# Kernel tuning notes

Measured on AMD Instinct MI355X. Metric: run time of the kernel, lower is better.

## Reference

```python
import jax, jax.numpy as jnp
import numpy as np

N_NODES = 50000
N_FEAT = 128
HIDDEN = 3
N_EDGES = 600000
N_POWERS = 3


def setup_inputs() -> dict:
    key = jax.random.key(0)
    ks = jax.random.split(key, 6)
    x = jax.random.normal(ks[0], (N_NODES, N_FEAT), dtype=jnp.float32)
    edge_index = jax.random.randint(ks[1], (N_POWERS, 2, N_EDGES), 0, N_NODES, dtype=jnp.int64)
    # MLP params for the 3 adjacency powers, stacked on the leading axis.
    # torch Linear(in,out) stored transposed here: y = x @ W + b.
    Wa = jax.random.normal(ks[2], (N_POWERS, N_FEAT, HIDDEN), dtype=jnp.float32) * (1.0 / np.sqrt(N_FEAT))
    ba = jax.random.normal(ks[3], (N_POWERS, HIDDEN), dtype=jnp.float32) * 0.01
    Wb = jax.random.normal(ks[4], (N_POWERS, HIDDEN, 1), dtype=jnp.float32) * (1.0 / np.sqrt(HIDDEN))
    bb = jax.random.normal(ks[5], (N_POWERS, 1), dtype=jnp.float32) * 0.01
    return {"x": x, "edge_index": edge_index, "Wa": Wa, "ba": ba, "Wb": Wb, "bb": bb}


def reference(x, edge_index, Wa, ba, Wb, bb):
    # Gather source/target node features per edge, per adjacency power.
    x_j = x[edge_index[:, 0]]          # [P, E, F]
    x_i = x[edge_index[:, 1]]          # [P, E, F]
    abs_dif = jnp.abs(x_j - x_i)       # [P, E, F]
    # Tiny per-edge MLP: Linear -> ReLU -> Linear -> Sigmoid (separate params per power).
    h = jax.nn.relu(jnp.einsum('pef,pfh->peh', abs_dif, Wa) + ba[:, None, :])  # [P, E, H]
    w = jax.nn.sigmoid(jnp.einsum('peh,pho->peo', h, Wb) + bb[:, None, :])     # [P, E, 1]
    return w[..., 0]                   # [P, E] edge weights for each power
```

## Files before the change

kernel.cpp:

```cpp
#include <hip/hip_runtime.h>
#include <math.h>

#define N_NODES 50000
#define N_FEAT  128
#define N_EDGES 600000
#define N_POWERS 3

#define PAIRS 5
#define EDGES_PER_BLK (64 * PAIRS)

#define CAP 81920
#define NBUCK 8
#define CHUNK 2048
#define NCHUNK 293

typedef _Float16 half2v __attribute__((ext_vector_type(2)));
union HU { unsigned u; half2v h; };

__device__ __forceinline__ int bucket_of(int j) { return (int)(((unsigned)j * 41u) >> 18); }

__global__ __launch_bounds__(256) void conv_x_plain(const float* __restrict__ x,
                                                    unsigned* __restrict__ xh,
                                                    const float* __restrict__ Wa,
                                                    unsigned* __restrict__ wah) {
    const int t = blockIdx.x * 256 + threadIdx.x;
    const float4* x4 = (const float4*)x;
    float4 a = x4[(size_t)t * 2];
    float4 b = x4[(size_t)t * 2 + 1];
    HU p0, p1, p2, p3;
    p0.h = half2v{(_Float16)a.x, (_Float16)a.y};
    p1.h = half2v{(_Float16)a.z, (_Float16)a.w};
    p2.h = half2v{(_Float16)b.x, (_Float16)b.y};
    p3.h = half2v{(_Float16)b.z, (_Float16)b.w};
    ((uint4*)xh)[t] = uint4{p0.u, p1.u, p2.u, p3.u};
    if (blockIdx.x == 0 && threadIdx.x < 192) {
        const int tt = threadIdx.x;
        #pragma unroll
        for (int q = 0; q < 3; ++q) {
            int idx = tt + q * 192;
            int c  = idx % 3;
            int pk = idx / 3;
            int k  = pk % 64;
            int p  = pk / 64;
            float w0 = Wa[p * 384 + (2 * k) * 3 + c];
            float w1 = Wa[p * 384 + (2 * k + 1) * 3 + c];
            HU u; u.h = half2v{(_Float16)w0, (_Float16)w1};
            wah[idx] = u.u;
        }
    }
}

__global__ __launch_bounds__(256) void hist_kernel(const int* __restrict__ edge_index,
                                                   int* __restrict__ hist) {
    __shared__ int lh[NBUCK];
    const int p = blockIdx.y, chunk = blockIdx.x;
    if (threadIdx.x < NBUCK) lh[threadIdx.x] = 0;
    __syncthreads();
    const int* ej = edge_index + (size_t)p * 2 * N_EDGES;
    const int base = chunk * CHUNK;
    #pragma unroll
    for (int k = 0; k < 8; ++k) {
        const int e = base + k * 256 + threadIdx.x;
        if (e < N_EDGES) {
            const int j = __builtin_nontemporal_load(ej + e);
            atomicAdd(&lh[bucket_of(j)], 1);
        }
    }
    __syncthreads();
    if (threadIdx.x < NBUCK)
        hist[(p * NBUCK + threadIdx.x) * NCHUNK + chunk] = lh[threadIdx.x];
}

__global__ __launch_bounds__(64) void scan_hist(int* __restrict__ hist,
                                                int* __restrict__ cur) {
    const int pb = blockIdx.x;
    const int lane = threadIdx.x;
    int* h = hist + pb * NCHUNK;
    int carry = 0;
    for (int t = 0; t < NCHUNK; t += 64) {
        const int c = t + lane;
        int v = (c < NCHUNK) ? h[c] : 0;
        int s = v;
        #pragma unroll
        for (int d = 1; d < 64; d <<= 1) {
            int u = __shfl_up(s, d, 64);
            if (lane >= d) s += u;
        }
        if (c < NCHUNK) h[c] = carry + (s - v);
        carry += __shfl(s, 63, 64);
    }
    if (lane == 0) cur[pb] = carry;
}

__global__ __launch_bounds__(256) void scatter_pass(const int* __restrict__ edge_index,
                                                    const int* __restrict__ hist,
                                                    unsigned long long* __restrict__ su) {
    __shared__ int lc[NBUCK];
    const int p = blockIdx.y, chunk = blockIdx.x;
    if (threadIdx.x < NBUCK) lc[threadIdx.x] = 0;
    __syncthreads();
    const int* ej = edge_index + (size_t)p * 2 * N_EDGES;
    const int* ei = ej + N_EDGES;
    const int base = chunk * CHUNK;
    #pragma unroll
    for (int k = 0; k < 8; ++k) {
        const int e = base + k * 256 + threadIdx.x;
        if (e < N_EDGES) {
            const int j = __builtin_nontemporal_load(ej + e);
            const int i = __builtin_nontemporal_load(ei + e);
            const int b = bucket_of(j);
            const int pos = atomicAdd(&lc[b], 1);
            const int off = hist[(p * NBUCK + b) * NCHUNK + chunk];
            const size_t slot = (size_t)(p * NBUCK + b) * CAP + off + pos;
            su[slot] = (unsigned long long)(unsigned)(j | (i << 16))
                     | ((unsigned long long)e << 32);
        }
    }
}

template<int PAT>
__device__ __forceinline__ float swz(float v) {
    return __int_as_float(__builtin_amdgcn_ds_swizzle(__float_as_int(v), PAT));
}

__device__ __forceinline__ void dot3_8(const uint4& qa0, const uint4& qa1,
                                       const uint4& qb0, const uint4& qb1,
                                       const HU wa[8][3],
                                       float& h0, float& h1, float& h2) {
    unsigned ua[8] = {qa0.x, qa0.y, qa0.z, qa0.w, qa1.x, qa1.y, qa1.z, qa1.w};
    unsigned ub[8] = {qb0.x, qb0.y, qb0.z, qb0.w, qb1.x, qb1.y, qb1.z, qb1.w};
    h0 = 0.f; h1 = 0.f; h2 = 0.f;
    #pragma unroll
    for (int k = 0; k < 8; ++k) {
        HU a, b, d;
        a.u = ua[k]; b.u = ub[k];
        d.h = a.h - b.h;
        d.u &= 0x7fff7fffu;
        h0 = __builtin_amdgcn_fdot2(d.h, wa[k][0].h, h0, false);
        h1 = __builtin_amdgcn_fdot2(d.h, wa[k][1].h, h1, false);
        h2 = __builtin_amdgcn_fdot2(d.h, wa[k][2].h, h2, false);
    }
}

__global__ __launch_bounds__(256) void adj_kernel_sorted(
    const unsigned* __restrict__ xh,
    const unsigned long long* __restrict__ su,
    const int* __restrict__ cur,
    const unsigned* __restrict__ wah,
    const float* __restrict__ ba,
    const float* __restrict__ Wb,
    const float* __restrict__ bb,
    float* __restrict__ out)
{
    const int p    = blockIdx.y;
    const int b    = blockIdx.x & 7;
    const int k    = blockIdx.x >> 3;
    const int tid  = threadIdx.x;
    const int lane = tid & 63;
    const int wave = tid >> 6;
    const int sub  = lane & 7;
    const int grp  = lane >> 3;

    const int count = cur[p * NBUCK + b];
    const int base  = k * EDGES_PER_BLK;
    if (base >= count) return;

    HU wa[8][3];
    {
        const unsigned* wp = wah + ((size_t)p * 64 + sub * 8) * 3;
        #pragma unroll
        for (int kk = 0; kk < 8; ++kk) {
            wa[kk][0].u = wp[kk * 3 + 0];
            wa[kk][1].u = wp[kk * 3 + 1];
            wa[kk][2].u = wp[kk * 3 + 2];
        }
        #pragma unroll
        for (int kk = 0; kk < 8; ++kk) {
            asm volatile("" : "+v"(wa[kk][0].u), "+v"(wa[kk][1].u), "+v"(wa[kk][2].u));
        }
    }

    const float ba0 = ba[p * 3 + 0], ba1 = ba[p * 3 + 1], ba2 = ba[p * 3 + 2];
    const float wb0 = Wb[p * 3 + 0], wb1 = Wb[p * 3 + 1], wb2 = Wb[p * 3 + 2];
    const float bbp = bb[p];

    const unsigned long long* sup = su + (size_t)(p * NBUCK + b) * CAP;
    float* outp = out + (size_t)p * N_EDGES;

    const int eoff = wave * 8 + grp;
    const int roff = sub * 8;
    const int cm1  = count - 1;

    #pragma unroll
    for (int it = 0; it < PAIRS; ++it) {
        const int r1 = base + it * 64 + eoff;
        const int r2 = r1 + 32;
        const bool v1 = r1 < count;
        const bool v2 = r2 < count;
        const int s1 = min(r1, cm1);
        const int s2 = min(r2, cm1);

        const unsigned long long q1 = __builtin_nontemporal_load(sup + s1);
        const unsigned long long q2 = __builtin_nontemporal_load(sup + s2);
        const int j1 = (int)(q1 & 0xFFFFu);
        const int i1 = (int)((q1 >> 16) & 0xFFFFu);
        const int e1 = (int)(q1 >> 32);
        const int j2 = (int)(q2 & 0xFFFFu);
        const int i2 = (int)((q2 >> 16) & 0xFFFFu);
        const int e2 = (int)(q2 >> 32);

        const uint4* rj1 = (const uint4*)(xh + ((size_t)j1 << 6) + roff);
        const uint4* ri1 = (const uint4*)(xh + ((size_t)i1 << 6) + roff);
        const uint4* rj2 = (const uint4*)(xh + ((size_t)j2 << 6) + roff);
        const uint4* ri2 = (const uint4*)(xh + ((size_t)i2 << 6) + roff);
        uint4 a0 = rj1[0], a1 = rj1[1];
        uint4 b0 = ri1[0], b1 = ri1[1];
        uint4 c0 = rj2[0], c1 = rj2[1];
        uint4 d0 = ri2[0], d1 = ri2[1];

        float h0a, h1a, h2a, h0b, h1b, h2b;
        dot3_8(a0, a1, b0, b1, wa, h0a, h1a, h2a);
        dot3_8(c0, c1, d0, d1, wa, h0b, h1b, h2b);

        h0a += swz<0x041F>(h0a); h1a += swz<0x041F>(h1a); h2a += swz<0x041F>(h2a);
        h0b += swz<0x041F>(h0b); h1b += swz<0x041F>(h1b); h2b += swz<0x041F>(h2b);
        h0a += swz<0x081F>(h0a); h1a += swz<0x081F>(h1a); h2a += swz<0x081F>(h2a);
        h0b += swz<0x081F>(h0b); h1b += swz<0x081F>(h1b); h2b += swz<0x081F>(h2b);
        h0a += swz<0x101F>(h0a); h1a += swz<0x101F>(h1a); h2a += swz<0x101F>(h2a);
        h0b += swz<0x101F>(h0b); h1b += swz<0x101F>(h1b); h2b += swz<0x101F>(h2b);

        if (sub == 0) {
            if (v1) {
                float r0 = fmaxf(h0a + ba0, 0.f);
                float r1f = fmaxf(h1a + ba1, 0.f);
                float r2f = fmaxf(h2a + ba2, 0.f);
                float s  = fmaf(r0, wb0, fmaf(r1f, wb1, fmaf(r2f, wb2, bbp)));
                __builtin_nontemporal_store(1.f / (1.f + __expf(-s)), outp + e1);
            }
            if (v2) {
                float r0 = fmaxf(h0b + ba0, 0.f);
                float r1f = fmaxf(h1b + ba1, 0.f);
                float r2f = fmaxf(h2b + ba2, 0.f);
                float s  = fmaf(r0, wb0, fmaf(r1f, wb1, fmaf(r2f, wb2, bbp)));
                __builtin_nontemporal_store(1.f / (1.f + __expf(-s)), outp + e2);
            }
        }
    }
}

__global__ __launch_bounds__(256) void adj_kernel_f16(
    const unsigned* __restrict__ xh,
    const unsigned* __restrict__ wah,
    const int*   __restrict__ edge_index,
    const float* __restrict__ ba,
    const float* __restrict__ Wb,
    const float* __restrict__ bb,
    float* __restrict__ out)
{
    const int p    = blockIdx.y;
    const int tid  = threadIdx.x;
    const int lane = tid & 63;
    const int wave = tid >> 6;
    const int sub  = lane & 7;
    const int grp  = lane >> 3;

    HU wa[8][3];
    {
        const unsigned* wp = wah + ((size_t)p * 64 + sub * 8) * 3;
        #pragma unroll
        for (int k = 0; k < 8; ++k) {
            wa[k][0].u = wp[k * 3 + 0];
            wa[k][1].u = wp[k * 3 + 1];
            wa[k][2].u = wp[k * 3 + 2];
        }
        #pragma unroll
        for (int k = 0; k < 8; ++k) {
            asm volatile("" : "+v"(wa[k][0].u), "+v"(wa[k][1].u), "+v"(wa[k][2].u));
        }
    }

    const float ba0 = ba[p * 3 + 0], ba1 = ba[p * 3 + 1], ba2 = ba[p * 3 + 2];
    const float wb0 = Wb[p * 3 + 0], wb1 = Wb[p * 3 + 1], wb2 = Wb[p * 3 + 2];
    const float bbp = bb[p];

    const int* ej = edge_index + (size_t)p * 2 * N_EDGES;
    const int* ei = ej + N_EDGES;
    float* outp = out + (size_t)p * N_EDGES;

    const int e_blk = blockIdx.x * EDGES_PER_BLK;
    const int eoff  = wave * 8 + grp;
    const int roff  = sub * 8;

    #pragma unroll
    for (int it = 0; it < PAIRS; ++it) {
        const int e1 = e_blk + it * 64 + eoff;
        const int e2 = e1 + 32;
        const int j1 = __builtin_nontemporal_load(ej + e1);
        const int i1 = __builtin_nontemporal_load(ei + e1);
        const int j2 = __builtin_nontemporal_load(ej + e2);
        const int i2 = __builtin_nontemporal_load(ei + e2);

        const uint4* rj1 = (const uint4*)(xh + ((size_t)j1 << 6) + roff);
        const uint4* ri1 = (const uint4*)(xh + ((size_t)i1 << 6) + roff);
        const uint4* rj2 = (const uint4*)(xh + ((size_t)j2 << 6) + roff);
        const uint4* ri2 = (const uint4*)(xh + ((size_t)i2 << 6) + roff);
        uint4 a0 = rj1[0], a1 = rj1[1];
        uint4 b0 = ri1[0], b1 = ri1[1];
        uint4 c0 = rj2[0], c1 = rj2[1];
        uint4 d0 = ri2[0], d1 = ri2[1];

        float h0a, h1a, h2a, h0b, h1b, h2b;
        dot3_8(a0, a1, b0, b1, wa, h0a, h1a, h2a);
        dot3_8(c0, c1, d0, d1, wa, h0b, h1b, h2b);

        h0a += swz<0x041F>(h0a); h1a += swz<0x041F>(h1a); h2a += swz<0x041F>(h2a);
        h0b += swz<0x041F>(h0b); h1b += swz<0x041F>(h1b); h2b += swz<0x041F>(h2b);
        h0a += swz<0x081F>(h0a); h1a += swz<0x081F>(h1a); h2a += swz<0x081F>(h2a);
        h0b += swz<0x081F>(h0b); h1b += swz<0x081F>(h1b); h2b += swz<0x081F>(h2b);
        h0a += swz<0x101F>(h0a); h1a += swz<0x101F>(h1a); h2a += swz<0x101F>(h2a);
        h0b += swz<0x101F>(h0b); h1b += swz<0x101F>(h1b); h2b += swz<0x101F>(h2b);

        if (sub == 0) {
            float r0 = fmaxf(h0a + ba0, 0.f);
            float r1 = fmaxf(h1a + ba1, 0.f);
            float r2 = fmaxf(h2a + ba2, 0.f);
            float s  = fmaf(r0, wb0, fmaf(r1, wb1, fmaf(r2, wb2, bbp)));
            __builtin_nontemporal_store(1.f / (1.f + __expf(-s)), outp + e1);
            r0 = fmaxf(h0b + ba0, 0.f);
            r1 = fmaxf(h1b + ba1, 0.f);
            r2 = fmaxf(h2b + ba2, 0.f);
            s  = fmaf(r0, wb0, fmaf(r1, wb1, fmaf(r2, wb2, bbp)));
            __builtin_nontemporal_store(1.f / (1.f + __expf(-s)), outp + e2);
        }
    }
}

__global__ __launch_bounds__(256) void adj_kernel_f32(
    const float* __restrict__ x,
    const int*   __restrict__ edge_index,
    const float* __restrict__ Wa,
    const float* __restrict__ ba,
    const float* __restrict__ Wb,
    const float* __restrict__ bb,
    float* __restrict__ out)
{
    const int p    = blockIdx.y;
    const int tid  = threadIdx.x;
    const int lane = tid & 63;
    const int wave = tid >> 6;
    const int sub  = lane & 15;
    const int grp  = lane >> 4;
    const int f0 = sub * 8;

    const float* Wap = Wa + (size_t)p * N_FEAT * 3;
    float wa0[8], wa1[8], wa2[8];
    #pragma unroll
    for (int k = 0; k < 8; ++k) {
        wa0[k] = Wap[(f0 + k) * 3 + 0];
        wa1[k] = Wap[(f0 + k) * 3 + 1];
        wa2[k] = Wap[(f0 + k) * 3 + 2];
    }
    const float ba0 = ba[p * 3 + 0], ba1 = ba[p * 3 + 1], ba2 = ba[p * 3 + 2];
    const float wb0 = Wb[p * 3 + 0], wb1 = Wb[p * 3 + 1], wb2 = Wb[p * 3 + 2];
    const float bbp = bb[p];

    const int e = blockIdx.x * 16 + wave * 4 + grp;
    const int* ej = edge_index + (size_t)p * 2 * N_EDGES;
    const int* ei = ej + N_EDGES;
    const int j = ej[e];
    const int i = ei[e];

    const float4* xj = (const float4*)(x + (size_t)j * N_FEAT + f0);
    const float4* xi = (const float4*)(x + (size_t)i * N_FEAT + f0);
    float4 a0 = xj[0], a1 = xj[1];
    float4 b0 = xi[0], b1 = xi[1];

    float d[8];
    d[0] = fabsf(a0.x - b0.x); d[1] = fabsf(a0.y - b0.y);
    d[2] = fabsf(a0.z - b0.z); d[3] = fabsf(a0.w - b0.w);
    d[4] = fabsf(a1.x - b1.x); d[5] = fabsf(a1.y - b1.y);
    d[6] = fabsf(a1.z - b1.z); d[7] = fabsf(a1.w - b1.w);

    float h0 = 0.f, h1 = 0.f, h2 = 0.f;
    #pragma unroll
    for (int k = 0; k < 8; ++k) {
        h0 = fmaf(d[k], wa0[k], h0);
        h1 = fmaf(d[k], wa1[k], h1);
        h2 = fmaf(d[k], wa2[k], h2);
    }
    #pragma unroll
    for (int m = 1; m < 16; m <<= 1) {
        h0 += __shfl_xor(h0, m, 64);
        h1 += __shfl_xor(h1, m, 64);
        h2 += __shfl_xor(h2, m, 64);
    }
    if (sub == 0) {
        float r0 = fmaxf(h0 + ba0, 0.f);
        float r1 = fmaxf(h1 + ba1, 0.f);
        float r2 = fmaxf(h2 + ba2, 0.f);
        float s  = fmaf(r0, wb0, fmaf(r1, wb1, fmaf(r2, wb2, bbp)));
        float w  = 1.f / (1.f + expf(-s));
        out[(size_t)p * N_EDGES + e] = w;
    }
}

extern "C" void kernel_launch(void* const* d_in, const int* in_sizes, int n_in,
                              void* d_out, int out_size, void* d_ws, size_t ws_size,
                              hipStream_t stream) {
    const float* x          = (const float*)d_in[0];
    const int*   edge_index = (const int*)d_in[1];
    const float* Wa         = (const float*)d_in[2];
    const float* ba         = (const float*)d_in[3];
    const float* Wb         = (const float*)d_in[4];
    const float* bb         = (const float*)d_in[5];
    float* out = (float*)d_out;

    const size_t x_bytes    = (size_t)N_NODES * N_FEAT * 2;
    const size_t su_bytes   = (size_t)N_POWERS * NBUCK * CAP * 8;
    const size_t wa_bytes   = 2304;
    const size_t hist_bytes = (size_t)N_POWERS * NBUCK * NCHUNK * 4;
    const size_t cur_bytes  = NBUCK * N_POWERS * 4;
    const size_t need_full  = x_bytes + su_bytes + wa_bytes + hist_bytes + cur_bytes;

    if (ws_size >= need_full) {
        char* w = (char*)d_ws;
        unsigned* xh = (unsigned*)w;
        unsigned long long* su = (unsigned long long*)(w + x_bytes);
        unsigned* wah = (unsigned*)(w + x_bytes + su_bytes);
        int* hist = (int*)(w + x_bytes + su_bytes + wa_bytes);
        int* cur  = (int*)(w + x_bytes + su_bytes + wa_bytes + hist_bytes);

        conv_x_plain<<<N_NODES * N_FEAT / 2048, 256, 0, stream>>>(x, xh, Wa, wah);
        hist_kernel<<<dim3(NCHUNK, N_POWERS), 256, 0, stream>>>(edge_index, hist);
        scan_hist<<<NBUCK * N_POWERS, 64, 0, stream>>>(hist, cur);
        scatter_pass<<<dim3(NCHUNK, N_POWERS), 256, 0, stream>>>(edge_index, hist, su);
        dim3 grid(NBUCK * (CAP / EDGES_PER_BLK), N_POWERS);
        adj_kernel_sorted<<<grid, 256, 0, stream>>>(xh, su, cur, wah, ba, Wb, bb, out);
    } else if (ws_size >= x_bytes + wa_bytes) {
        unsigned* xh  = (unsigned*)d_ws;
        unsigned* wah = (unsigned*)((char*)d_ws + x_bytes);
        conv_x_plain<<<N_NODES * N_FEAT / 2048, 256, 0, stream>>>(x, xh, Wa, wah);
        dim3 grid(N_EDGES / EDGES_PER_BLK, N_POWERS);
        adj_kernel_f16<<<grid, 256, 0, stream>>>(xh, wah, edge_index, ba, Wb, bb, out);
    } else {
        dim3 grid((N_EDGES + 15) / 16, N_POWERS);
        adj_kernel_f32<<<grid, 256, 0, stream>>>(x, edge_index, Wa, ba, Wb, bb, out);
    }
}
```

Baseline: 177.1 us.

## Replace fdot2 edge MLP with MFMA 16x16x32 f16 tiles over sorted edges

Swaps the sorted-edge kernel's packed-fp16 dot products for MFMA 16x16x32 f16 instructions. Each wave handles 16 edges per tile and accumulates the 128-feature |xj-xi| times padded Wa (3 columns padded to 16) in matrix cores. The sorted-edge record for the next tile is prefetched, and sigmoid outputs go through shared memory for coalesced stores. This cuts the swizzle-reduction and ALU work, at the cost of padded MFMA columns, extra weight preparation, and an LDS round trip per tile.

```diff
diff --git a/kernel.cpp b/kernel.cpp
--- a/kernel.cpp
+++ b/kernel.cpp
@@ -6,23 +6,27 @@
 #define N_EDGES 600000
 #define N_POWERS 3
 
-#define PAIRS 5
-#define EDGES_PER_BLK (64 * PAIRS)
-
 #define CAP 81920
 #define NBUCK 8
 #define CHUNK 2048
 #define NCHUNK 293
 
+#define TILES 10
+#define EDGES_PER_BLK (4 * TILES * 16)
+
 typedef _Float16 half2v __attribute__((ext_vector_type(2)));
+typedef _Float16 half8  __attribute__((ext_vector_type(8)));
+typedef float    f32x4  __attribute__((ext_vector_type(4)));
 union HU { unsigned u; half2v h; };
+union BU { unsigned u[4]; half8 h; };
 
 __device__ __forceinline__ int bucket_of(int j) { return (int)(((unsigned)j * 41u) >> 18); }
 
 __global__ __launch_bounds__(256) void conv_x_plain(const float* __restrict__ x,
                                                     unsigned* __restrict__ xh,
                                                     const float* __restrict__ Wa,
-                                                    unsigned* __restrict__ wah) {
+                                                    unsigned* __restrict__ wah,
+                                                    unsigned* __restrict__ waf) {
     const int t = blockIdx.x * 256 + threadIdx.x;
     const float4* x4 = (const float4*)x;
     float4 a = x4[(size_t)t * 2];
@@ -33,19 +37,34 @@
     p2.h = half2v{(_Float16)b.x, (_Float16)b.y};
     p3.h = half2v{(_Float16)b.z, (_Float16)b.w};
     ((uint4*)xh)[t] = uint4{p0.u, p1.u, p2.u, p3.u};
-    if (blockIdx.x == 0 && threadIdx.x < 192) {
-        const int tt = threadIdx.x;
-        #pragma unroll
-        for (int q = 0; q < 3; ++q) {
-            int idx = tt + q * 192;
-            int c  = idx % 3;
-            int pk = idx / 3;
-            int k  = pk % 64;
-            int p  = pk / 64;
-            float w0 = Wa[p * 384 + (2 * k) * 3 + c];
-            float w1 = Wa[p * 384 + (2 * k + 1) * 3 + c];
+    if (blockIdx.x == 0) {
+        if (threadIdx.x < 192) {
+            const int tt = threadIdx.x;
+            #pragma unroll
+            for (int q = 0; q < 3; ++q) {
+                int idx = tt + q * 192;
+                int c  = idx % 3;
+                int pk = idx / 3;
+                int k  = pk % 64;
+                int p  = pk / 64;
+                float w0 = Wa[p * 384 + (2 * k) * 3 + c];
+                float w1 = Wa[p * 384 + (2 * k + 1) * 3 + c];
+                HU u; u.h = half2v{(_Float16)w0, (_Float16)w1};
+                wah[idx] = u.u;
+            }
+        }
+        for (int w = threadIdx.x; w < 3072; w += 256) {
+            int kk = w & 63;
+            int pn = w >> 6;
+            int n  = pn & 15;
+            int p  = pn >> 4;
+            float w0 = 0.f, w1 = 0.f;
+            if (n < 3) {
+                w0 = Wa[p * 384 + (2 * kk) * 3 + n];
+                w1 = Wa[p * 384 + (2 * kk + 1) * 3 + n];
+            }
             HU u; u.h = half2v{(_Float16)w0, (_Float16)w1};
-            wah[idx] = u.u;
+            waf[w] = u.u;
         }
     }
 }
@@ -112,8 +131,8 @@
             const int pos = atomicAdd(&lc[b], 1);
             const int off = hist[(p * NBUCK + b) * NCHUNK + chunk];
             const size_t slot = (size_t)(p * NBUCK + b) * CAP + off + pos;
-            su[slot] = (unsigned long long)(unsigned)(j | (i << 16))
-                     | ((unsigned long long)e << 32);
+            su[slot] = (unsigned long long)(((unsigned)i << 16) | (unsigned)j)
+                     | ((unsigned long long)(unsigned)e << 32);
         }
     }
 }
@@ -121,6 +140,115 @@
 template<int PAT>
 __device__ __forceinline__ float swz(float v) {
     return __int_as_float(__builtin_amdgcn_ds_swizzle(__float_as_int(v), PAT));
+}
+
+__device__ __forceinline__ half8 mk_d(uint4 qa, uint4 qb) {
+    BU d;
+    {
+        HU a, b, r;
+        a.u = qa.x; b.u = qb.x; r.h = a.h - b.h; d.u[0] = r.u & 0x7fff7fffu;
+        a.u = qa.y; b.u = qb.y; r.h = a.h - b.h; d.u[1] = r.u & 0x7fff7fffu;
+        a.u = qa.z; b.u = qb.z; r.h = a.h - b.h; d.u[2] = r.u & 0x7fff7fffu;
+        a.u = qa.w; b.u = qb.w; r.h = a.h - b.h; d.u[3] = r.u & 0x7fff7fffu;
+    }
+    return d.h;
+}
+
+__global__ __launch_bounds__(256) void adj_kernel_mfma(
+    const unsigned* __restrict__ xh,
+    const unsigned long long* __restrict__ su,
+    const int* __restrict__ cur,
+    const unsigned* __restrict__ waf,
+    const float* __restrict__ ba,
+    const float* __restrict__ Wb,
+    const float* __restrict__ bb,
+    float* __restrict__ out)
+{
+    __shared__ float lw[64];
+
+    const int p    = blockIdx.y;
+    const int b    = blockIdx.x & 7;
+    const int kblk = blockIdx.x >> 3;
+    const int tid  = threadIdx.x;
+    const int lane = tid & 63;
+    const int wave = tid >> 6;
+    const int c    = lane & 15;
+    const int quad = lane >> 4;
+
+    const int count = cur[p * NBUCK + b];
+    const int base  = kblk * EDGES_PER_BLK;
+    if (base >= count) return;
+
+    BU bf[4];
+    {
+        const unsigned* wp = waf + (size_t)(p * 16 + c) * 64 + quad * 4;
+        #pragma unroll
+        for (int ks = 0; ks < 4; ++ks) {
+            bf[ks].u[0] = wp[ks * 16 + 0];
+            bf[ks].u[1] = wp[ks * 16 + 1];
+            bf[ks].u[2] = wp[ks * 16 + 2];
+            bf[ks].u[3] = wp[ks * 16 + 3];
+        }
+        #pragma unroll
+        for (int ks = 0; ks < 4; ++ks)
+            asm volatile("" : "+v"(bf[ks].u[0]), "+v"(bf[ks].u[1]),
+                              "+v"(bf[ks].u[2]), "+v"(bf[ks].u[3]));
+    }
+
+    const float ba0 = ba[p * 3 + 0], ba1 = ba[p * 3 + 1], ba2 = ba[p * 3 + 2];
+    const float wb0 = Wb[p * 3 + 0], wb1 = Wb[p * 3 + 1], wb2 = Wb[p * 3 + 2];
+    const float bbp = bb[p];
+    const float ba_v = (c == 0) ? ba0 : ((c == 1) ? ba1 : ((c == 2) ? ba2 : 0.f));
+    const float wb_v = (c == 0) ? wb0 : ((c == 1) ? wb1 : ((c == 2) ? wb2 : 0.f));
+
+    const unsigned long long* sup = su + (size_t)(p * NBUCK + b) * CAP;
+    float* outp = out + (size_t)p * N_EDGES;
+    const int cm1 = count - 1;
+
+    int tb = base + wave * 16;
+    unsigned long long q = sup[min(tb + c, cm1)];
+
+    #pragma unroll 2
+    for (int t = 0; t < TILES; ++t) {
+        const int tbt = base + wave * 16 + t * 64;
+        const int j = (int)(q & 0xFFFFu);
+        const int i = (int)((q >> 16) & 0xFFFFu);
+        const int e = (int)(q >> 32);
+
+        const uint4* rj = (const uint4*)(xh + ((size_t)j << 6)) + quad;
+        const uint4* ri = (const uint4*)(xh + ((size_t)i << 6)) + quad;
+
+        unsigned long long qn = q;
+        if (t + 1 < TILES) qn = sup[min(tbt + 64 + c, cm1)];
+
+        f32x4 C = {0.f, 0.f, 0.f, 0.f};
+        #pragma unroll
+        for (int ks = 0; ks < 4; ++ks) {
+            uint4 qa = rj[ks * 4];
+            uint4 qb = ri[ks * 4];
+            C = __builtin_amdgcn_mfma_f32_16x16x32_f16(mk_d(qa, qb), bf[ks].h, C, 0, 0, 0);
+        }
+
+        float val[4];
+        #pragma unroll
+        for (int r = 0; r < 4; ++r) {
+            val[r] = fmaxf(C[r] + ba_v, 0.f) * wb_v;
+            val[r] += swz<0x041F>(val[r]);
+            val[r] += swz<0x081F>(val[r]);
+        }
+        if (c == 0) {
+            #pragma unroll
+            for (int r = 0; r < 4; ++r) {
+                float s = val[r] + bbp;
+                lw[wave * 16 + quad * 4 + r] = 1.f / (1.f + __expf(-s));
+            }
+        }
+        float wv = lw[wave * 16 + c];
+        if (quad == 0 && (tbt + c) < count)
+            __builtin_nontemporal_store(wv, outp + e);
+
+        q = qn;
+    }
 }
 
 __device__ __forceinline__ void dot3_8(const uint4& qa0, const uint4& qa1,
@@ -139,112 +267,6 @@
         h0 = __builtin_amdgcn_fdot2(d.h, wa[k][0].h, h0, false);
         h1 = __builtin_amdgcn_fdot2(d.h, wa[k][1].h, h1, false);
         h2 = __builtin_amdgcn_fdot2(d.h, wa[k][2].h, h2, false);
-    }
-}
-
-__global__ __launch_bounds__(256) void adj_kernel_sorted(
-    const unsigned* __restrict__ xh,
-    const unsigned long long* __restrict__ su,
-    const int* __restrict__ cur,
-    const unsigned* __restrict__ wah,
-    const float* __restrict__ ba,
-    const float* __restrict__ Wb,
-    const float* __restrict__ bb,
-    float* __restrict__ out)
-{
-    const int p    = blockIdx.y;
-    const int b    = blockIdx.x & 7;
-    const int k    = blockIdx.x >> 3;
-    const int tid  = threadIdx.x;
-    const int lane = tid & 63;
-    const int wave = tid >> 6;
-    const int sub  = lane & 7;
-    const int grp  = lane >> 3;
-
-    const int count = cur[p * NBUCK + b];
-    const int base  = k * EDGES_PER_BLK;
-    if (base >= count) return;
-
-    HU wa[8][3];
-    {
-        const unsigned* wp = wah + ((size_t)p * 64 + sub * 8) * 3;
-        #pragma unroll
-        for (int kk = 0; kk < 8; ++kk) {
-            wa[kk][0].u = wp[kk * 3 + 0];
-            wa[kk][1].u = wp[kk * 3 + 1];
-            wa[kk][2].u = wp[kk * 3 + 2];
-        }
-        #pragma unroll
-        for (int kk = 0; kk < 8; ++kk) {
-            asm volatile("" : "+v"(wa[kk][0].u), "+v"(wa[kk][1].u), "+v"(wa[kk][2].u));
-        }
-    }
-
-    const float ba0 = ba[p * 3 + 0], ba1 = ba[p * 3 + 1], ba2 = ba[p * 3 + 2];
-    const float wb0 = Wb[p * 3 + 0], wb1 = Wb[p * 3 + 1], wb2 = Wb[p * 3 + 2];
-    const float bbp = bb[p];
-
-    const unsigned long long* sup = su + (size_t)(p * NBUCK + b) * CAP;
-    float* outp = out + (size_t)p * N_EDGES;
-
-    const int eoff = wave * 8 + grp;
-    const int roff = sub * 8;
-    const int cm1  = count - 1;
-
-    #pragma unroll
-    for (int it = 0; it < PAIRS; ++it) {
-        const int r1 = base + it * 64 + eoff;
-        const int r2 = r1 + 32;
-        const bool v1 = r1 < count;
-        const bool v2 = r2 < count;
-        const int s1 = min(r1, cm1);
-        const int s2 = min(r2, cm1);
-
-        const unsigned long long q1 = __builtin_nontemporal_load(sup + s1);
-        const unsigned long long q2 = __builtin_nontemporal_load(sup + s2);
-        const int j1 = (int)(q1 & 0xFFFFu);
-        const int i1 = (int)((q1 >> 16) & 0xFFFFu);
-        const int e1 = (int)(q1 >> 32);
-        const int j2 = (int)(q2 & 0xFFFFu);
-        const int i2 = (int)((q2 >> 16) & 0xFFFFu);
-        const int e2 = (int)(q2 >> 32);
-
-        const uint4* rj1 = (const uint4*)(xh + ((size_t)j1 << 6) + roff);
-        const uint4* ri1 = (const uint4*)(xh + ((size_t)i1 << 6) + roff);
-        const uint4* rj2 = (const uint4*)(xh + ((size_t)j2 << 6) + roff);
-        const uint4* ri2 = (const uint4*)(xh + ((size_t)i2 << 6) + roff);
-        uint4 a0 = rj1[0], a1 = rj1[1];
-        uint4 b0 = ri1[0], b1 = ri1[1];
-        uint4 c0 = rj2[0], c1 = rj2[1];
-        uint4 d0 = ri2[0], d1 = ri2[1];
-
-        float h0a, h1a, h2a, h0b, h1b, h2b;
-        dot3_8(a0, a1, b0, b1, wa, h0a, h1a, h2a);
-        dot3_8(c0, c1, d0, d1, wa, h0b, h1b, h2b);
-
-        h0a += swz<0x041F>(h0a); h1a += swz<0x041F>(h1a); h2a += swz<0x041F>(h2a);
-        h0b += swz<0x041F>(h0b); h1b += swz<0x041F>(h1b); h2b += swz<0x041F>(h2b);
-        h0a += swz<0x081F>(h0a); h1a += swz<0x081F>(h1a); h2a += swz<0x081F>(h2a);
-        h0b += swz<0x081F>(h0b); h1b += swz<0x081F>(h1b); h2b += swz<0x081F>(h2b);
-        h0a += swz<0x101F>(h0a); h1a += swz<0x101F>(h1a); h2a += swz<0x101F>(h2a);
-        h0b += swz<0x101F>(h0b); h1b += swz<0x101F>(h1b); h2b += swz<0x101F>(h2b);
-
-        if (sub == 0) {
-            if (v1) {
-                float r0 = fmaxf(h0a + ba0, 0.f);
-                float r1f = fmaxf(h1a + ba1, 0.f);
-                float r2f = fmaxf(h2a + ba2, 0.f);
-                float s  = fmaf(r0, wb0, fmaf(r1f, wb1, fmaf(r2f, wb2, bbp)));
-                __builtin_nontemporal_store(1.f / (1.f + __expf(-s)), outp + e1);
-            }
-            if (v2) {
-                float r0 = fmaxf(h0b + ba0, 0.f);
-                float r1f = fmaxf(h1b + ba1, 0.f);
-                float r2f = fmaxf(h2b + ba2, 0.f);
-                float s  = fmaf(r0, wb0, fmaf(r1f, wb1, fmaf(r2f, wb2, bbp)));
-                __builtin_nontemporal_store(1.f / (1.f + __expf(-s)), outp + e2);
-            }
-        }
     }
 }
 
@@ -274,9 +296,8 @@
             wa[k][2].u = wp[k * 3 + 2];
         }
         #pragma unroll
-        for (int k = 0; k < 8; ++k) {
+        for (int k = 0; k < 8; ++k)
             asm volatile("" : "+v"(wa[k][0].u), "+v"(wa[k][1].u), "+v"(wa[k][2].u));
-        }
     }
 
     const float ba0 = ba[p * 3 + 0], ba1 = ba[p * 3 + 1], ba2 = ba[p * 3 + 2];
@@ -287,12 +308,12 @@
     const int* ei = ej + N_EDGES;
     float* outp = out + (size_t)p * N_EDGES;
 
-    const int e_blk = blockIdx.x * EDGES_PER_BLK;
+    const int e_blk = blockIdx.x * 320;
     const int eoff  = wave * 8 + grp;
     const int roff  = sub * 8;
 
     #pragma unroll
-    for (int it = 0; it < PAIRS; ++it) {
+    for (int it = 0; it < 5; ++it) {
         const int e1 = e_blk + it * 64 + eoff;
         const int e2 = e1 + 32;
         const int j1 = __builtin_nontemporal_load(ej + e1);
@@ -417,30 +438,33 @@
 
     const size_t x_bytes    = (size_t)N_NODES * N_FEAT * 2;
     const size_t su_bytes   = (size_t)N_POWERS * NBUCK * CAP * 8;
-    const size_t wa_bytes   = 2304;
+    const size_t wah_bytes  = 2304;
+    const size_t waf_bytes  = 12288;
     const size_t hist_bytes = (size_t)N_POWERS * NBUCK * NCHUNK * 4;
     const size_t cur_bytes  = NBUCK * N_POWERS * 4;
-    const size_t need_full  = x_bytes + su_bytes + wa_bytes + hist_bytes + cur_bytes;
+    const size_t need_full  = x_bytes + su_bytes + wah_bytes + waf_bytes + hist_bytes + cur_bytes;
 
     if (ws_size >= need_full) {
         char* w = (char*)d_ws;
         unsigned* xh = (unsigned*)w;
         unsigned long long* su = (unsigned long long*)(w + x_bytes);
         unsigned* wah = (unsigned*)(w + x_bytes + su_bytes);
-        int* hist = (int*)(w + x_bytes + su_bytes + wa_bytes);
-        int* cur  = (int*)(w + x_bytes + su_bytes + wa_bytes + hist_bytes);
-
-        conv_x_plain<<<N_NODES * N_FEAT / 2048, 256, 0, stream>>>(x, xh, Wa, wah);
+        unsigned* waf = (unsigned*)(w + x_bytes + su_bytes + wah_bytes);
+        int* hist = (int*)(w + x_bytes + su_bytes + wah_bytes + waf_bytes);
+        int* cur  = (int*)(w + x_bytes + su_bytes + wah_bytes + waf_bytes + hist_bytes);
+
+        conv_x_plain<<<N_NODES * N_FEAT / 2048, 256, 0, stream>>>(x, xh, Wa, wah, waf);
         hist_kernel<<<dim3(NCHUNK, N_POWERS), 256, 0, stream>>>(edge_index, hist);
         scan_hist<<<NBUCK * N_POWERS, 64, 0, stream>>>(hist, cur);
         scatter_pass<<<dim3(NCHUNK, N_POWERS), 256, 0, stream>>>(edge_index, hist, su);
         dim3 grid(NBUCK * (CAP / EDGES_PER_BLK), N_POWERS);
-        adj_kernel_sorted<<<grid, 256, 0, stream>>>(xh, su, cur, wah, ba, Wb, bb, out);
-    } else if (ws_size >= x_bytes + wa_bytes) {
+        adj_kernel_mfma<<<grid, 256, 0, stream>>>(xh, su, cur, waf, ba, Wb, bb, out);
+    } else if (ws_size >= x_bytes + wah_bytes + waf_bytes) {
         unsigned* xh  = (unsigned*)d_ws;
         unsigned* wah = (unsigned*)((char*)d_ws + x_bytes);
-        conv_x_plain<<<N_NODES * N_FEAT / 2048, 256, 0, stream>>>(x, xh, Wa, wah);
-        dim3 grid(N_EDGES / EDGES_PER_BLK, N_POWERS);
+        unsigned* waf = (unsigned*)((char*)d_ws + x_bytes + wah_bytes);
+        conv_x_plain<<<N_NODES * N_FEAT / 2048, 256, 0, stream>>>(x, xh, Wa, wah, waf);
+        dim3 grid(N_EDGES / 320, N_POWERS);
         adj_kernel_f16<<<grid, 256, 0, stream>>>(xh, wah, edge_index, ba, Wb, bb, out);
     } else {
         dim3 grid((N_EDGES + 15) / 16, N_POWERS);
```

New measurement: 225.5 us. +27.3%, slower.

## Bucket edges by both source and target node slices for gather locality

Applied to the files above, without the earlier changes.

Edges are now binned into an 8x8 grid of source-slice by target-slice buckets (64 per power) instead of 8 source-only buckets. The goal is that each block's gathers of both endpoint rows fall within a small slice of the fp16 feature table, so they hit in L2. With the grid ordering, blockIdx.x & 7 pins a source slice per XCD under round-robin dispatch. In exchange, the histogram pass now also reads target indices and uses 64 shared counters, the scan grows, and per-bucket capacity is tighter (10240), with a guard that drops edges if a bucket overflows.

```diff
diff --git a/kernel.cpp b/kernel.cpp
--- a/kernel.cpp
+++ b/kernel.cpp
@@ -6,18 +6,19 @@
 #define N_EDGES 600000
 #define N_POWERS 3
 
-#define PAIRS 5
-#define EDGES_PER_BLK (64 * PAIRS)
-
-#define CAP 81920
-#define NBUCK 8
+#define NJB 8
+#define NIB 8
+#define NB64 64
+#define CAP64 10240
 #define CHUNK 2048
 #define NCHUNK 293
 
+#define EDGES_PER_BLK 320
+
 typedef _Float16 half2v __attribute__((ext_vector_type(2)));
 union HU { unsigned u; half2v h; };
 
-__device__ __forceinline__ int bucket_of(int j) { return (int)(((unsigned)j * 41u) >> 18); }
+__device__ __forceinline__ int slice_of(int v) { return (int)(((unsigned)v * 41u) >> 18); }
 
 __global__ __launch_bounds__(256) void conv_x_plain(const float* __restrict__ x,
                                                     unsigned* __restrict__ xh,
@@ -52,23 +53,25 @@
 
 __global__ __launch_bounds__(256) void hist_kernel(const int* __restrict__ edge_index,
                                                    int* __restrict__ hist) {
-    __shared__ int lh[NBUCK];
+    __shared__ int lh[NB64];
     const int p = blockIdx.y, chunk = blockIdx.x;
-    if (threadIdx.x < NBUCK) lh[threadIdx.x] = 0;
+    if (threadIdx.x < NB64) lh[threadIdx.x] = 0;
     __syncthreads();
     const int* ej = edge_index + (size_t)p * 2 * N_EDGES;
+    const int* ei = ej + N_EDGES;
     const int base = chunk * CHUNK;
     #pragma unroll
     for (int k = 0; k < 8; ++k) {
         const int e = base + k * 256 + threadIdx.x;
         if (e < N_EDGES) {
             const int j = __builtin_nontemporal_load(ej + e);
-            atomicAdd(&lh[bucket_of(j)], 1);
+            const int i = __builtin_nontemporal_load(ei + e);
+            atomicAdd(&lh[slice_of(j) * NIB + slice_of(i)], 1);
         }
     }
     __syncthreads();
-    if (threadIdx.x < NBUCK)
-        hist[(p * NBUCK + threadIdx.x) * NCHUNK + chunk] = lh[threadIdx.x];
+    if (threadIdx.x < NB64)
+        hist[(p * NB64 + threadIdx.x) * NCHUNK + chunk] = lh[threadIdx.x];
 }
 
 __global__ __launch_bounds__(64) void scan_hist(int* __restrict__ hist,
@@ -95,9 +98,9 @@
 __global__ __launch_bounds__(256) void scatter_pass(const int* __restrict__ edge_index,
                                                     const int* __restrict__ hist,
                                                     unsigned long long* __restrict__ su) {
-    __shared__ int lc[NBUCK];
+    __shared__ int lc[NB64];
     const int p = blockIdx.y, chunk = blockIdx.x;
-    if (threadIdx.x < NBUCK) lc[threadIdx.x] = 0;
+    if (threadIdx.x < NB64) lc[threadIdx.x] = 0;
     __syncthreads();
     const int* ej = edge_index + (size_t)p * 2 * N_EDGES;
     const int* ei = ej + N_EDGES;
@@ -108,12 +111,14 @@
         if (e < N_EDGES) {
             const int j = __builtin_nontemporal_load(ej + e);
             const int i = __builtin_nontemporal_load(ei + e);
-            const int b = bucket_of(j);
+            const int b = slice_of(j) * NIB + slice_of(i);
             const int pos = atomicAdd(&lc[b], 1);
-            const int off = hist[(p * NBUCK + b) * NCHUNK + chunk];
-            const size_t slot = (size_t)(p * NBUCK + b) * CAP + off + pos;
-            su[slot] = (unsigned long long)(unsigned)(j | (i << 16))
-                     | ((unsigned long long)e << 32);
+            const int off = hist[(p * NB64 + b) * NCHUNK + chunk] + pos;
+            if (off < CAP64) {
+                const size_t slot = (size_t)(p * NB64 + b) * CAP64 + off;
+                su[slot] = (unsigned long long)(((unsigned)i << 16) | (unsigned)j)
+                         | ((unsigned long long)(unsigned)e << 32);
+            }
         }
     }
 }
@@ -142,7 +147,7 @@
     }
 }
 
-__global__ __launch_bounds__(256) void adj_kernel_sorted(
+__global__ __launch_bounds__(256) void adj_kernel_f16s(
     const unsigned* __restrict__ xh,
     const unsigned long long* __restrict__ su,
     const int* __restrict__ cur,
@@ -152,39 +157,41 @@
     const float* __restrict__ bb,
     float* __restrict__ out)
 {
-    const int p    = blockIdx.y;
-    const int b    = blockIdx.x & 7;
-    const int k    = blockIdx.x >> 3;
+    const int p      = blockIdx.y;
+    const int jb     = blockIdx.x & 7;
+    const int within = blockIdx.x >> 3;
+    const int ib     = within >> 5;
+    const int kblk   = within & 31;
     const int tid  = threadIdx.x;
     const int lane = tid & 63;
     const int wave = tid >> 6;
     const int sub  = lane & 7;
     const int grp  = lane >> 3;
 
-    const int count = cur[p * NBUCK + b];
-    const int base  = k * EDGES_PER_BLK;
+    const int bidx  = (p * NJB + jb) * NIB + ib;
+    const int count = min(cur[bidx], CAP64);
+    const int base  = kblk * EDGES_PER_BLK;
     if (base >= count) return;
 
     HU wa[8][3];
     {
         const unsigned* wp = wah + ((size_t)p * 64 + sub * 8) * 3;
         #pragma unroll
-        for (int kk = 0; kk < 8; ++kk) {
-            wa[kk][0].u = wp[kk * 3 + 0];
-            wa[kk][1].u = wp[kk * 3 + 1];
-            wa[kk][2].u = wp[kk * 3 + 2];
-        }
-        #pragma unroll
-        for (int kk = 0; kk < 8; ++kk) {
-            asm volatile("" : "+v"(wa[kk][0].u), "+v"(wa[kk][1].u), "+v"(wa[kk][2].u));
-        }
+        for (int k = 0; k < 8; ++k) {
+            wa[k][0].u = wp[k * 3 + 0];
+            wa[k][1].u = wp[k * 3 + 1];
+            wa[k][2].u = wp[k * 3 + 2];
+        }
+        #pragma unroll
+        for (int k = 0; k < 8; ++k)
+            asm volatile("" : "+v"(wa[k][0].u), "+v"(wa[k][1].u), "+v"(wa[k][2].u));
     }
 
     const float ba0 = ba[p * 3 + 0], ba1 = ba[p * 3 + 1], ba2 = ba[p * 3 + 2];
     const float wb0 = Wb[p * 3 + 0], wb1 = Wb[p * 3 + 1], wb2 = Wb[p * 3 + 2];
     const float bbp = bb[p];
 
-    const unsigned long long* sup = su + (size_t)(p * NBUCK + b) * CAP;
+    const unsigned long long* sup = su + (size_t)bidx * CAP64;
     float* outp = out + (size_t)p * N_EDGES;
 
     const int eoff = wave * 8 + grp;
@@ -192,16 +199,14 @@
     const int cm1  = count - 1;
 
     #pragma unroll
-    for (int it = 0; it < PAIRS; ++it) {
+    for (int it = 0; it < 5; ++it) {
         const int r1 = base + it * 64 + eoff;
         const int r2 = r1 + 32;
         const bool v1 = r1 < count;
         const bool v2 = r2 < count;
-        const int s1 = min(r1, cm1);
-        const int s2 = min(r2, cm1);
-
-        const unsigned long long q1 = __builtin_nontemporal_load(sup + s1);
-        const unsigned long long q2 = __builtin_nontemporal_load(sup + s2);
+
+        const unsigned long long q1 = __builtin_nontemporal_load(sup + min(r1, cm1));
+        const unsigned long long q2 = __builtin_nontemporal_load(sup + min(r2, cm1));
         const int j1 = (int)(q1 & 0xFFFFu);
         const int i1 = (int)((q1 >> 16) & 0xFFFFu);
         const int e1 = (int)(q1 >> 32);
@@ -274,9 +279,8 @@
             wa[k][2].u = wp[k * 3 + 2];
         }
         #pragma unroll
-        for (int k = 0; k < 8; ++k) {
+        for (int k = 0; k < 8; ++k)
             asm volatile("" : "+v"(wa[k][0].u), "+v"(wa[k][1].u), "+v"(wa[k][2].u));
-        }
     }
 
     const float ba0 = ba[p * 3 + 0], ba1 = ba[p * 3 + 1], ba2 = ba[p * 3 + 2];
@@ -287,12 +291,12 @@
     const int* ei = ej + N_EDGES;
     float* outp = out + (size_t)p * N_EDGES;
 
-    const int e_blk = blockIdx.x * EDGES_PER_BLK;
+    const int e_blk = blockIdx.x * 320;
     const int eoff  = wave * 8 + grp;
     const int roff  = sub * 8;
 
     #pragma unroll
-    for (int it = 0; it < PAIRS; ++it) {
+    for (int it = 0; it < 5; ++it) {
         const int e1 = e_blk + it * 64 + eoff;
         const int e2 = e1 + 32;
         const int j1 = __builtin_nontemporal_load(ej + e1);
@@ -416,31 +420,31 @@
     float* out = (float*)d_out;
 
     const size_t x_bytes    = (size_t)N_NODES * N_FEAT * 2;
-    const size_t su_bytes   = (size_t)N_POWERS * NBUCK * CAP * 8;
-    const size_t wa_bytes   = 2304;
-    const size_t hist_bytes = (size_t)N_POWERS * NBUCK * NCHUNK * 4;
-    const size_t cur_bytes  = NBUCK * N_POWERS * 4;
-    const size_t need_full  = x_bytes + su_bytes + wa_bytes + hist_bytes + cur_bytes;
+    const size_t su_bytes   = (size_t)N_POWERS * NB64 * CAP64 * 8;
+    const size_t wah_bytes  = 2304;
+    const size_t hist_bytes = (size_t)N_POWERS * NB64 * NCHUNK * 4;
+    const size_t cur_bytes  = NB64 * N_POWERS * 4;
+    const size_t need_full  = x_bytes + su_bytes + wah_bytes + hist_bytes + cur_bytes;
 
     if (ws_size >= need_full) {
         char* w = (char*)d_ws;
         unsigned* xh = (unsigned*)w;
         unsigned long long* su = (unsigned long long*)(w + x_bytes);
         unsigned* wah = (unsigned*)(w + x_bytes + su_bytes);
-        int* hist = (int*)(w + x_bytes + su_bytes + wa_bytes);
-        int* cur  = (int*)(w + x_bytes + su_bytes + wa_bytes + hist_bytes);
+        int* hist = (int*)(w + x_bytes + su_bytes + wah_bytes);
+        int* cur  = (int*)(w + x_bytes + su_bytes + wah_bytes + hist_bytes);
 
         conv_x_plain<<<N_NODES * N_FEAT / 2048, 256, 0, stream>>>(x, xh, Wa, wah);
         hist_kernel<<<dim3(NCHUNK, N_POWERS), 256, 0, stream>>>(edge_index, hist);
-        scan_hist<<<NBUCK * N_POWERS, 64, 0, stream>>>(hist, cur);
+        scan_hist<<<NB64 * N_POWERS, 64, 0, stream>>>(hist, cur);
         scatter_pass<<<dim3(NCHUNK, N_POWERS), 256, 0, stream>>>(edge_index, hist, su);
-        dim3 grid(NBUCK * (CAP / EDGES_PER_BLK), N_POWERS);
-        adj_kernel_sorted<<<grid, 256, 0, stream>>>(xh, su, cur, wah, ba, Wb, bb, out);
-    } else if (ws_size >= x_bytes + wa_bytes) {
+        dim3 grid(NJB * NIB * (CAP64 / EDGES_PER_BLK), N_POWERS);
+        adj_kernel_f16s<<<grid, 256, 0, stream>>>(xh, su, cur, wah, ba, Wb, bb, out);
+    } else if (ws_size >= x_bytes + wah_bytes) {
         unsigned* xh  = (unsigned*)d_ws;
         unsigned* wah = (unsigned*)((char*)d_ws + x_bytes);
         conv_x_plain<<<N_NODES * N_FEAT / 2048, 256, 0, stream>>>(x, xh, Wa, wah);
-        dim3 grid(N_EDGES / EDGES_PER_BLK, N_POWERS);
+        dim3 grid(N_EDGES / 320, N_POWERS);
         adj_kernel_f16<<<grid, 256, 0, stream>>>(xh, wah, edge_index, ba, Wb, bb, out);
     } else {
         dim3 grid((N_EDGES + 15) / 16, N_POWERS);
```

New measurement: 198.0 us. 1.12x slower.
